# Performance work log

Measured on AMD Instinct MI355X. Metric: run time of the kernel, lower is better.

Reference implementation:

```python
import jax, jax.numpy as jnp
import numpy as np

D = 2048
H = 16
KV = 4
DH = D // H  # 128
REP = H // KV
ROPE_BASE = 10000.0


def _rope(x, pos):
    # x: (B, h, L, Dh), pos: (L,)
    half = x.shape[-1] // 2
    inv_freq = 1.0 / (ROPE_BASE ** (jnp.arange(0, half, dtype=jnp.float32) / half))
    ang = pos.astype(jnp.float32)[:, None] * inv_freq[None, :]          # (L, half)
    cos = jnp.concatenate([jnp.cos(ang), jnp.cos(ang)], axis=-1)        # (L, Dh)
    sin = jnp.concatenate([jnp.sin(ang), jnp.sin(ang)], axis=-1)
    x1, x2 = x[..., :half], x[..., half:]
    rot = jnp.concatenate([-x2, x1], axis=-1)
    return x * cos[None, None] + rot * sin[None, None]


def setup_inputs() -> dict:
    key = jax.random.key(0)
    ks = jax.random.split(key, 5)
    s = 1.0 / np.sqrt(D)
    return {
        "x": jax.random.normal(ks[0], (2, 2048, D), dtype=jnp.float32),
        "wq": jax.random.uniform(ks[1], (H * DH, D), jnp.float32, -s, s),
        "wk": jax.random.uniform(ks[2], (KV * DH, D), jnp.float32, -s, s),
        "wv": jax.random.uniform(ks[3], (KV * DH, D), jnp.float32, -s, s),
        "wo": jax.random.uniform(ks[4], (D, H * DH), jnp.float32, -s, s),
    }


def reference(x, wq, wk, wv, wo):
    B, T, _ = x.shape
    q = (x @ wq.T).reshape(B, T, H, DH).transpose(0, 2, 1, 3)    # (B,H,T,Dh)
    k = (x @ wk.T).reshape(B, T, KV, DH).transpose(0, 2, 1, 3)   # (B,KV,T,Dh)
    v = (x @ wv.T).reshape(B, T, KV, DH).transpose(0, 2, 1, 3)
    Tc = T  # no kv cache
    pos = jnp.arange(Tc)
    q = _rope(q, pos)
    k = _rope(k, pos)
    # GQA: repeat kv heads to match query heads
    k_full = jnp.repeat(k, REP, axis=1)                          # (B,H,Tc,Dh)
    v_full = jnp.repeat(v, REP, axis=1)
    scale = 1.0 / np.sqrt(DH)
    scores = jnp.einsum('bhtd,bhsd->bhts', q, k_full) * scale    # (B,H,T,Tc)
    row = jnp.arange(T)[:, None]
    col = jnp.arange(Tc)[None, :]
    causal = col <= row + (Tc - T)
    scores = jnp.where(causal[None, None], scores, -jnp.inf)
    attn = jax.nn.softmax(scores, axis=-1)
    out = jnp.einsum('bhts,bhsd->bhtd', attn, v_full)            # (B,H,T,Dh)
    out = out.transpose(0, 2, 1, 3).reshape(B, T, H * DH)
    return out @ wo.T
```

## Files before the change

kernel.cpp:

```cpp
#include <hip/hip_runtime.h>

typedef float f32x4 __attribute__((ext_vector_type(4)));
typedef short s16x8 __attribute__((ext_vector_type(8)));
typedef unsigned short u16;

__device__ __forceinline__ u16 f2bf(float f) {
    union { float f; unsigned u; } v; v.f = f;
    return (u16)((v.u + 0x7fffu + ((v.u >> 16) & 1u)) >> 16);
}
__device__ __forceinline__ float bf2f(u16 h) {
    union { unsigned u; float f; } v; v.u = ((unsigned)h) << 16;
    return v.f;
}
__device__ __forceinline__ float fast_exp2(float x) {
#if __has_builtin(__builtin_amdgcn_exp2f)
    return __builtin_amdgcn_exp2f(x);
#else
    return exp2f(x);
#endif
}

__device__ __forceinline__ void gload_lds16(const void* g, void* l) {
    __builtin_amdgcn_global_load_lds((__attribute__((address_space(1))) void*)g,
                                     (__attribute__((address_space(3))) void*)l, 16, 0, 0);
}

__global__ __launch_bounds__(256) void cvt_all(const float* __restrict__ x,  const float* __restrict__ wq,
                                               const float* __restrict__ wk, const float* __restrict__ wv,
                                               u16* __restrict__ xb, u16* __restrict__ wqkvb) {
    int u = blockIdx.x * 256 + threadIdx.x;
    const float* src;
    u16* dst;
    if (u < 1048576) { src = x + (size_t)u * 8; dst = xb + (size_t)u * 8; }
    else {
        int w = u - 1048576;
        dst = wqkvb + (size_t)w * 8;
        if (w < 524288)      src = wq + (size_t)w * 8;
        else if (w < 655360) src = wk + (size_t)(w - 524288) * 8;
        else                 src = wv + (size_t)(w - 655360) * 8;
    }
    const float4* p = (const float4*)src;
    float4 a = p[0], b = p[1];
    s16x8 o;
    o[0] = f2bf(a.x); o[1] = f2bf(a.y); o[2] = f2bf(a.z); o[3] = f2bf(a.w);
    o[4] = f2bf(b.x); o[5] = f2bf(b.y); o[6] = f2bf(b.z); o[7] = f2bf(b.w);
    *(s16x8*)dst = o;
}

__global__ __launch_bounds__(256) void cvt_kernel(const float* __restrict__ in,
                                                  u16* __restrict__ out, int n8) {
    int i = blockIdx.x * 256 + threadIdx.x;
    if (i >= n8) return;
    const float4* p = (const float4*)(in + (size_t)i * 8);
    float4 a = p[0], b = p[1];
    s16x8 o;
    o[0] = f2bf(a.x); o[1] = f2bf(a.y); o[2] = f2bf(a.z); o[3] = f2bf(a.w);
    o[4] = f2bf(b.x); o[5] = f2bf(b.y); o[6] = f2bf(b.z); o[7] = f2bf(b.w);
    *(s16x8*)(out + (size_t)i * 8) = o;
}

template<int OUT>
__global__ __launch_bounds__(256) void gemm128(const u16* __restrict__ A, const u16* __restrict__ B,
                                               void* __restrict__ C, void* __restrict__ Ck,
                                               void* __restrict__ Cv, int M, int N, int K) {
    __shared__ __align__(16) u16 Ald[128 * 64];
    __shared__ __align__(16) u16 Bld[128 * 64];
    const int t = threadIdx.x, wid = t >> 6, lane = t & 63;
    const int m0 = blockIdx.y * 128, n0 = blockIdx.x * 128;
    const int ml = lane & 15, quad = lane >> 4, m7 = ml & 7;
    const int wm = (wid & 1) * 64, wn = (wid >> 1) * 64;
    const int sr = lane >> 3, sc = lane & 7;

    f32x4 acc[4][4] = {};

    for (int k0 = 0; k0 < K; k0 += 64) {
        if (k0) __syncthreads();
        #pragma unroll
        for (int i = 0; i < 4; ++i) {
            int seg = wid * 4 + i;
            int r = seg * 8 + sr;
            int c = (sc ^ (r & 7)) * 8;
            gload_lds16(A + (size_t)(m0 + r) * K + k0 + c, &Ald[seg * 512]);
            gload_lds16(B + (size_t)(n0 + r) * K + k0 + c, &Bld[seg * 512]);
        }
        __syncthreads();
        #pragma unroll
        for (int kk = 0; kk < 64; kk += 32) {
            s16x8 af[4], bf[4];
            #pragma unroll
            for (int mi = 0; mi < 4; ++mi)
                af[mi] = *(const s16x8*)&Ald[(wm + mi * 16 + ml) * 64 + (((kk >> 3) + quad) ^ m7) * 8];
            #pragma unroll
            for (int ni = 0; ni < 4; ++ni)
                bf[ni] = *(const s16x8*)&Bld[(wn + ni * 16 + ml) * 64 + (((kk >> 3) + quad) ^ m7) * 8];
            #pragma unroll
            for (int mi = 0; mi < 4; ++mi)
                #pragma unroll
                for (int ni = 0; ni < 4; ++ni)
                    acc[mi][ni] = __builtin_amdgcn_mfma_f32_16x16x32_bf16(af[mi], bf[ni], acc[mi][ni], 0, 0, 0);
        }
    }
    #pragma unroll
    for (int mi = 0; mi < 4; ++mi)
        #pragma unroll
        for (int ni = 0; ni < 4; ++ni) {
            int gmb = m0 + wm + mi * 16 + quad * 4;
            int gn  = n0 + wn + ni * 16 + ml;
            if constexpr (OUT == 4) {
                if (n0 < 2048) {
                    #pragma unroll
                    for (int r = 0; r < 4; ++r)
                        ((u16*)C)[(size_t)(gmb + r) * 2048 + gn] = f2bf(acc[mi][ni][r]);
                } else if (n0 < 2560) {
                    #pragma unroll
                    for (int r = 0; r < 4; ++r)
                        ((u16*)Ck)[(size_t)(gmb + r) * 512 + (gn - 2048)] = f2bf(acc[mi][ni][r]);
                } else {
                    ushort4 v;
                    v.x = f2bf(acc[mi][ni][0]); v.y = f2bf(acc[mi][ni][1]);
                    v.z = f2bf(acc[mi][ni][2]); v.w = f2bf(acc[mi][ni][3]);
                    *(ushort4*)((u16*)Cv + (size_t)(gn - 2560) * M + gmb) = v;
                }
            } else {
                #pragma unroll
                for (int r = 0; r < 4; ++r)
                    ((float*)C)[(size_t)(gmb + r) * N + gn] = acc[mi][ni][r];
            }
        }
}

__global__ __launch_bounds__(256) void rope_kernel(u16* __restrict__ qb, u16* __restrict__ kb,
                                                   int nq, int ntot, float sq) {
    int idx = blockIdx.x * 256 + threadIdx.x;
    if (idx >= ntot) return;
    u16* base; int nheads; float scl; int id;
    if (idx < nq) { base = qb; nheads = 16; scl = sq;  id = idx; }
    else          { base = kb; nheads = 4;  scl = 1.f; id = idx - nq; }
    int i = id & 63;
    int rest = id >> 6;
    int hh = rest % nheads;
    int tok = rest / nheads;
    int tpos = tok & 2047;
    u16* row = base + (size_t)tok * nheads * 128 + hh * 128;
    float x1 = bf2f(row[i]);
    float x2 = bf2f(row[i + 64]);
    float inv = expf(-(float)i * 0.14391156731570787f);
    float ang = (float)tpos * inv;
    float s, c;
    sincosf(ang, &s, &c);
    row[i]      = f2bf((x1 * c - x2 * s) * scl);
    row[i + 64] = f2bf((x2 * c + x1 * s) * scl);
}

__global__ __launch_bounds__(256, 2) void attn_kernel(const u16* __restrict__ Q, const u16* __restrict__ Kb,
                                                      const u16* __restrict__ Vt, u16* __restrict__ O) {
    __shared__ __align__(16) u16 Klds[64 * 128];
    __shared__ __align__(16) u16 Vlds[128 * 64];
    __shared__ __align__(16) u16 Plds[4][2][16 * 64];
    const int t = threadIdx.x, wslot = t >> 6, lane = t & 63;
    const int qa = blockIdx.x, qb = 127 - (int)blockIdx.x;
    const int kv = blockIdx.y, b = blockIdx.z;
    const int h = kv * 4 + wslot;
    const int ml = lane & 15, quad = lane >> 4, m7 = ml & 7;
    const int t0a = qa * 16, t0b = qb * 16;

    s16x8 qfA[4], qfB[4];
    {
        const u16* qpA = Q + ((size_t)(b * 2048 + t0a + ml) * 2048 + h * 128);
        const u16* qpB = Q + ((size_t)(b * 2048 + t0b + ml) * 2048 + h * 128);
        #pragma unroll
        for (int kc = 0; kc < 4; ++kc) {
            qfA[kc] = *(const s16x8*)(qpA + kc * 32 + quad * 8);
            qfB[kc] = *(const s16x8*)(qpB + kc * 32 + quad * 8);
        }
    }

    s16x8 ones;
    #pragma unroll
    for (int j = 0; j < 8; ++j) ones[j] = (short)0x3F80;

    f32x4 OA[8] = {}, OB[8] = {};
    f32x4 LA = {}, LB = {};

    const int nsb = (qb >> 2) + 1;
    const int lastA = qa >> 2;

    for (int it = 0; it < nsb; ++it) {
        const int s0 = it * 64;
        if (it) __syncthreads();
        #pragma unroll
        for (int i = 0; i < 4; ++i) {
            int seg = wslot * 4 + i;
            int kr = seg * 4 + (lane >> 4);
            int kc = ((lane & 15) ^ (kr & 7)) * 8;
            gload_lds16(Kb + (size_t)(b * 2048 + s0 + kr) * 512 + kv * 128 + kc, &Klds[seg * 512]);
            int vr = seg * 8 + (lane >> 3);
            int vc = ((lane & 7) ^ (vr & 7)) * 8;
            gload_lds16(Vt + (size_t)(kv * 128 + vr) * 4096 + b * 2048 + s0 + vc, &Vlds[seg * 512]);
        }
        __syncthreads();

        const bool actA = (it <= lastA);

        f32x4 Sa[4] = {}, Sb[4] = {};
        if (actA) {
            #pragma unroll
            for (int kc = 0; kc < 4; ++kc)
                #pragma unroll
                for (int ti = 0; ti < 4; ++ti) {
                    s16x8 kf = *(const s16x8*)&Klds[(ti * 16 + ml) * 128 + ((kc * 4 + quad) ^ m7) * 8];
                    Sb[ti] = __builtin_amdgcn_mfma_f32_16x16x32_bf16(qfB[kc], kf, Sb[ti], 0, 0, 0);
                    Sa[ti] = __builtin_amdgcn_mfma_f32_16x16x32_bf16(qfA[kc], kf, Sa[ti], 0, 0, 0);
                }
        } else {
            #pragma unroll
            for (int kc = 0; kc < 4; ++kc)
                #pragma unroll
                for (int ti = 0; ti < 4; ++ti) {
                    s16x8 kf = *(const s16x8*)&Klds[(ti * 16 + ml) * 128 + ((kc * 4 + quad) ^ m7) * 8];
                    Sb[ti] = __builtin_amdgcn_mfma_f32_16x16x32_bf16(qfB[kc], kf, Sb[ti], 0, 0, 0);
                }
        }

        auto do_soft = [&](f32x4* S, int t0, int pslot) {
            u16* pl = &Plds[wslot][pslot][0];
            #pragma unroll
            for (int r = 0; r < 4; ++r) {
                int qr = t0 + quad * 4 + r;
                int row = quad * 4 + r;
                #pragma unroll
                for (int ti = 0; ti < 4; ++ti) {
                    float e = fast_exp2(S[ti][r]);
                    if (s0 + ti * 16 + ml > qr) e = 0.f;
                    union { float f; unsigned u; } cv; cv.f = e;
                    pl[row * 64 + (((ti * 2 + (ml >> 3)) ^ (row & 7)) * 8) + (ml & 7)] = (u16)(cv.u >> 16);
                }
            }
        };
        do_soft(Sb, t0b, 1);
        if (actA) do_soft(Sa, t0a, 0);
        asm volatile("s_waitcnt lgkmcnt(0)" ::: "memory");
        s16x8 pfA[2], pfB[2];
        pfB[0] = *(const s16x8*)&Plds[wslot][1][ml * 64 + ((quad)     ^ m7) * 8];
        pfB[1] = *(const s16x8*)&Plds[wslot][1][ml * 64 + ((4 + quad) ^ m7) * 8];
        if (actA) {
            pfA[0] = *(const s16x8*)&Plds[wslot][0][ml * 64 + ((quad)     ^ m7) * 8];
            pfA[1] = *(const s16x8*)&Plds[wslot][0][ml * 64 + ((4 + quad) ^ m7) * 8];
        }
        asm volatile("s_waitcnt lgkmcnt(0)" ::: "memory");

        if (actA) {
            #pragma unroll
            for (int c = 0; c < 2; ++c) {
                #pragma unroll
                for (int nt = 0; nt < 8; ++nt) {
                    s16x8 vf = *(const s16x8*)&Vlds[(nt * 16 + ml) * 64 + ((c * 4 + quad) ^ m7) * 8];
                    OB[nt] = __builtin_amdgcn_mfma_f32_16x16x32_bf16(pfB[c], vf, OB[nt], 0, 0, 0);
                    OA[nt] = __builtin_amdgcn_mfma_f32_16x16x32_bf16(pfA[c], vf, OA[nt], 0, 0, 0);
                }
                LB = __builtin_amdgcn_mfma_f32_16x16x32_bf16(pfB[c], ones, LB, 0, 0, 0);
                LA = __builtin_amdgcn_mfma_f32_16x16x32_bf16(pfA[c], ones, LA, 0, 0, 0);
            }
        } else {
            #pragma unroll
            for (int c = 0; c < 2; ++c) {
                #pragma unroll
                for (int nt = 0; nt < 8; ++nt) {
                    s16x8 vf = *(const s16x8*)&Vlds[(nt * 16 + ml) * 64 + ((c * 4 + quad) ^ m7) * 8];
                    OB[nt] = __builtin_amdgcn_mfma_f32_16x16x32_bf16(pfB[c], vf, OB[nt], 0, 0, 0);
                }
                LB = __builtin_amdgcn_mfma_f32_16x16x32_bf16(pfB[c], ones, LB, 0, 0, 0);
            }
        }
    }

    #pragma unroll
    for (int nt = 0; nt < 8; ++nt)
        #pragma unroll
        for (int r = 0; r < 4; ++r) {
            int col = h * 128 + nt * 16 + ml;
            O[(size_t)(b * 2048 + t0b + quad * 4 + r) * 2048 + col] = f2bf(OB[nt][r] / LB[r]);
            O[(size_t)(b * 2048 + t0a + quad * 4 + r) * 2048 + col] = f2bf(OA[nt][r] / LA[r]);
        }
}

extern "C" void kernel_launch(void* const* d_in, const int* in_sizes, int n_in,
                              void* d_out, int out_size, void* d_ws, size_t ws_size,
                              hipStream_t stream) {
    const float* x  = (const float*)d_in[0];
    const float* wq = (const float*)d_in[1];
    const float* wk = (const float*)d_in[2];
    const float* wv = (const float*)d_in[3];
    const float* wo = (const float*)d_in[4];
    float* out = (float*)d_out;
    char* ws = (char*)d_ws;

    const size_t MB = 1024 * 1024;
    u16* xb    = (u16*)(ws);
    u16* qb    = (u16*)(ws + 16 * MB);
    u16* kb    = (u16*)(ws + 32 * MB);
    u16* vtb   = (u16*)(ws + 36 * MB);
    u16* wqkvb = (u16*)(ws + 40 * MB);
    u16* ab    = xb;
    u16* wob   = wqkvb;

    cvt_all<<<7168, 256, 0, stream>>>(x, wq, wk, wv, xb, wqkvb);

    gemm128<4><<<dim3(24, 32), 256, 0, stream>>>(xb, wqkvb, qb, kb, vtb, 4096, 3072, 2048);

    cvt_kernel<<<2048, 256, 0, stream>>>(wo, wob, 524288);

    rope_kernel<<<20480, 256, 0, stream>>>(qb, kb, 4194304, 5242880, 0.12751743f);

    attn_kernel<<<dim3(64, 4, 2), 256, 0, stream>>>(qb, kb, vtb, ab);

    gemm128<1><<<dim3(16, 32), 256, 0, stream>>>(ab, wob, out, nullptr, nullptr, 4096, 2048, 2048);
}
```

Before: 336.0 us.

## Split paired query tiles into one tile per block with staggered ordering

The attention kernel no longer gives each block a pair of complementary query tiles (qa, 127-qa) for load balance. Each block now handles a single 16-row query tile, the grid doubles to 128 blocks in x, and the tile order is permuted per (kv,batch) group to spread long and short tiles across the machine. Launch bounds go from 2 to 4 blocks per SIMD-group target, and the causal mask is applied only on the diagonal iteration. This raises block count and occupancy and cuts register pressure. In exchange, K/V tiles loaded into LDS are reused by one query tile instead of two, so shared-memory load traffic per MFMA roughly doubles.

```diff
diff --git a/kernel.cpp b/kernel.cpp
--- a/kernel.cpp
+++ b/kernel.cpp
@@ -152,40 +152,43 @@
     row[i + 64] = f2bf((x2 * c + x1 * s) * scl);
 }
 
-__global__ __launch_bounds__(256, 2) void attn_kernel(const u16* __restrict__ Q, const u16* __restrict__ Kb,
+__global__ __launch_bounds__(256, 4) void attn_kernel(const u16* __restrict__ Q, const u16* __restrict__ Kb,
                                                       const u16* __restrict__ Vt, u16* __restrict__ O) {
     __shared__ __align__(16) u16 Klds[64 * 128];
     __shared__ __align__(16) u16 Vlds[128 * 64];
-    __shared__ __align__(16) u16 Plds[4][2][16 * 64];
+    __shared__ __align__(16) u16 Plds[4][16 * 64];
     const int t = threadIdx.x, wslot = t >> 6, lane = t & 63;
-    const int qa = blockIdx.x, qb = 127 - (int)blockIdx.x;
     const int kv = blockIdx.y, b = blockIdx.z;
+    const int g = kv + 4 * b;
+    const int bx = blockIdx.x;
+    int qt;
+    switch ((g >> 1) & 3) {
+        case 0:  qt = bx; break;
+        case 1:  qt = 127 - bx; break;
+        case 2:  qt = (bx + 64) & 127; break;
+        default: qt = (63 - bx) & 127; break;
+    }
     const int h = kv * 4 + wslot;
     const int ml = lane & 15, quad = lane >> 4, m7 = ml & 7;
-    const int t0a = qa * 16, t0b = qb * 16;
-
-    s16x8 qfA[4], qfB[4];
+    const int t0 = qt * 16;
+    const int n = (qt >> 2) + 1;
+
+    s16x8 qf[4];
     {
-        const u16* qpA = Q + ((size_t)(b * 2048 + t0a + ml) * 2048 + h * 128);
-        const u16* qpB = Q + ((size_t)(b * 2048 + t0b + ml) * 2048 + h * 128);
-        #pragma unroll
-        for (int kc = 0; kc < 4; ++kc) {
-            qfA[kc] = *(const s16x8*)(qpA + kc * 32 + quad * 8);
-            qfB[kc] = *(const s16x8*)(qpB + kc * 32 + quad * 8);
-        }
+        const u16* qp = Q + ((size_t)(b * 2048 + t0 + ml) * 2048 + h * 128);
+        #pragma unroll
+        for (int kc = 0; kc < 4; ++kc)
+            qf[kc] = *(const s16x8*)(qp + kc * 32 + quad * 8);
     }
 
     s16x8 ones;
     #pragma unroll
     for (int j = 0; j < 8; ++j) ones[j] = (short)0x3F80;
 
-    f32x4 OA[8] = {}, OB[8] = {};
-    f32x4 LA = {}, LB = {};
-
-    const int nsb = (qb >> 2) + 1;
-    const int lastA = qa >> 2;
-
-    for (int it = 0; it < nsb; ++it) {
+    f32x4 Oa[8] = {};
+    f32x4 L = {};
+
+    for (int it = 0; it < n; ++it) {
         const int s0 = it * 64;
         if (it) __syncthreads();
         #pragma unroll
@@ -200,30 +203,18 @@
         }
         __syncthreads();
 
-        const bool actA = (it <= lastA);
-
-        f32x4 Sa[4] = {}, Sb[4] = {};
-        if (actA) {
-            #pragma unroll
-            for (int kc = 0; kc < 4; ++kc)
-                #pragma unroll
-                for (int ti = 0; ti < 4; ++ti) {
-                    s16x8 kf = *(const s16x8*)&Klds[(ti * 16 + ml) * 128 + ((kc * 4 + quad) ^ m7) * 8];
-                    Sb[ti] = __builtin_amdgcn_mfma_f32_16x16x32_bf16(qfB[kc], kf, Sb[ti], 0, 0, 0);
-                    Sa[ti] = __builtin_amdgcn_mfma_f32_16x16x32_bf16(qfA[kc], kf, Sa[ti], 0, 0, 0);
-                }
-        } else {
-            #pragma unroll
-            for (int kc = 0; kc < 4; ++kc)
-                #pragma unroll
-                for (int ti = 0; ti < 4; ++ti) {
-                    s16x8 kf = *(const s16x8*)&Klds[(ti * 16 + ml) * 128 + ((kc * 4 + quad) ^ m7) * 8];
-                    Sb[ti] = __builtin_amdgcn_mfma_f32_16x16x32_bf16(qfB[kc], kf, Sb[ti], 0, 0, 0);
-                }
-        }
-
-        auto do_soft = [&](f32x4* S, int t0, int pslot) {
-            u16* pl = &Plds[wslot][pslot][0];
+        f32x4 S[4] = {};
+        #pragma unroll
+        for (int kc = 0; kc < 4; ++kc)
+            #pragma unroll
+            for (int ti = 0; ti < 4; ++ti) {
+                s16x8 kf = *(const s16x8*)&Klds[(ti * 16 + ml) * 128 + ((kc * 4 + quad) ^ m7) * 8];
+                S[ti] = __builtin_amdgcn_mfma_f32_16x16x32_bf16(qf[kc], kf, S[ti], 0, 0, 0);
+            }
+
+        {
+            u16* pl = &Plds[wslot][0];
+            const bool diag = (it == n - 1);
             #pragma unroll
             for (int r = 0; r < 4; ++r) {
                 int qr = t0 + quad * 4 + r;
@@ -231,46 +222,26 @@
                 #pragma unroll
                 for (int ti = 0; ti < 4; ++ti) {
                     float e = fast_exp2(S[ti][r]);
-                    if (s0 + ti * 16 + ml > qr) e = 0.f;
+                    if (diag && (s0 + ti * 16 + ml > qr)) e = 0.f;
                     union { float f; unsigned u; } cv; cv.f = e;
                     pl[row * 64 + (((ti * 2 + (ml >> 3)) ^ (row & 7)) * 8) + (ml & 7)] = (u16)(cv.u >> 16);
                 }
             }
-        };
-        do_soft(Sb, t0b, 1);
-        if (actA) do_soft(Sa, t0a, 0);
+        }
         asm volatile("s_waitcnt lgkmcnt(0)" ::: "memory");
-        s16x8 pfA[2], pfB[2];
-        pfB[0] = *(const s16x8*)&Plds[wslot][1][ml * 64 + ((quad)     ^ m7) * 8];
-        pfB[1] = *(const s16x8*)&Plds[wslot][1][ml * 64 + ((4 + quad) ^ m7) * 8];
-        if (actA) {
-            pfA[0] = *(const s16x8*)&Plds[wslot][0][ml * 64 + ((quad)     ^ m7) * 8];
-            pfA[1] = *(const s16x8*)&Plds[wslot][0][ml * 64 + ((4 + quad) ^ m7) * 8];
-        }
+        s16x8 pf[2];
+        pf[0] = *(const s16x8*)&Plds[wslot][ml * 64 + ((quad)     ^ m7) * 8];
+        pf[1] = *(const s16x8*)&Plds[wslot][ml * 64 + ((4 + quad) ^ m7) * 8];
         asm volatile("s_waitcnt lgkmcnt(0)" ::: "memory");
 
-        if (actA) {
-            #pragma unroll
-            for (int c = 0; c < 2; ++c) {
-                #pragma unroll
-                for (int nt = 0; nt < 8; ++nt) {
-                    s16x8 vf = *(const s16x8*)&Vlds[(nt * 16 + ml) * 64 + ((c * 4 + quad) ^ m7) * 8];
-                    OB[nt] = __builtin_amdgcn_mfma_f32_16x16x32_bf16(pfB[c], vf, OB[nt], 0, 0, 0);
-                    OA[nt] = __builtin_amdgcn_mfma_f32_16x16x32_bf16(pfA[c], vf, OA[nt], 0, 0, 0);
-                }
-                LB = __builtin_amdgcn_mfma_f32_16x16x32_bf16(pfB[c], ones, LB, 0, 0, 0);
-                LA = __builtin_amdgcn_mfma_f32_16x16x32_bf16(pfA[c], ones, LA, 0, 0, 0);
-            }
-        } else {
-            #pragma unroll
-            for (int c = 0; c < 2; ++c) {
-                #pragma unroll
-                for (int nt = 0; nt < 8; ++nt) {
-                    s16x8 vf = *(const s16x8*)&Vlds[(nt * 16 + ml) * 64 + ((c * 4 + quad) ^ m7) * 8];
-                    OB[nt] = __builtin_amdgcn_mfma_f32_16x16x32_bf16(pfB[c], vf, OB[nt], 0, 0, 0);
-                }
-                LB = __builtin_amdgcn_mfma_f32_16x16x32_bf16(pfB[c], ones, LB, 0, 0, 0);
-            }
+        #pragma unroll
+        for (int c = 0; c < 2; ++c) {
+            #pragma unroll
+            for (int nt = 0; nt < 8; ++nt) {
+                s16x8 vf = *(const s16x8*)&Vlds[(nt * 16 + ml) * 64 + ((c * 4 + quad) ^ m7) * 8];
+                Oa[nt] = __builtin_amdgcn_mfma_f32_16x16x32_bf16(pf[c], vf, Oa[nt], 0, 0, 0);
+            }
+            L = __builtin_amdgcn_mfma_f32_16x16x32_bf16(pf[c], ones, L, 0, 0, 0);
         }
     }
 
@@ -279,8 +250,7 @@
         #pragma unroll
         for (int r = 0; r < 4; ++r) {
             int col = h * 128 + nt * 16 + ml;
-            O[(size_t)(b * 2048 + t0b + quad * 4 + r) * 2048 + col] = f2bf(OB[nt][r] / LB[r]);
-            O[(size_t)(b * 2048 + t0a + quad * 4 + r) * 2048 + col] = f2bf(OA[nt][r] / LA[r]);
+            O[(size_t)(b * 2048 + t0 + quad * 4 + r) * 2048 + col] = f2bf(Oa[nt][r] / L[r]);
         }
 }
 
@@ -312,7 +282,7 @@
 
     rope_kernel<<<20480, 256, 0, stream>>>(qb, kb, 4194304, 5242880, 0.12751743f);
 
-    attn_kernel<<<dim3(64, 4, 2), 256, 0, stream>>>(qb, kb, vtb, ab);
+    attn_kernel<<<dim3(128, 4, 2), 256, 0, stream>>>(qb, kb, vtb, ab);
 
     gemm128<1><<<dim3(16, 32), 256, 0, stream>>>(ab, wob, out, nullptr, nullptr, 4096, 2048, 2048);
 }
```

Measured after the change: 334.6 us. No clear change (-0.4%).

## Load K/V fragments directly from global memory instead of staging through LDS

Applied to the files above, without the earlier changes.

The attention kernel stops cooperatively staging K and V tiles into shared memory and drops the per-iteration block barriers. Each wave now reads its K and V MFMA fragments straight from global memory, relying on L1/L2 for reuse across the four waves of a block. The grid is flattened so the 8 (kv, batch) groups sharing a query-tile index are interleaved, which should improve cache locality, and the causal mask is applied only on the diagonal tile. The trade is more global load instructions and redundant per-wave traffic in exchange for removing LDS round trips and synchronisation.

```diff
diff --git a/kernel.cpp b/kernel.cpp
--- a/kernel.cpp
+++ b/kernel.cpp
@@ -154,15 +154,18 @@
 
 __global__ __launch_bounds__(256, 2) void attn_kernel(const u16* __restrict__ Q, const u16* __restrict__ Kb,
                                                       const u16* __restrict__ Vt, u16* __restrict__ O) {
-    __shared__ __align__(16) u16 Klds[64 * 128];
-    __shared__ __align__(16) u16 Vlds[128 * 64];
     __shared__ __align__(16) u16 Plds[4][2][16 * 64];
     const int t = threadIdx.x, wslot = t >> 6, lane = t & 63;
-    const int qa = blockIdx.x, qb = 127 - (int)blockIdx.x;
-    const int kv = blockIdx.y, b = blockIdx.z;
+    const int bid = blockIdx.x;
+    const int g = bid & 7;
+    const int u = bid >> 3;
+    const int kv = g & 3, b = g >> 2;
+    const int qa = u, qb = 127 - u;
     const int h = kv * 4 + wslot;
     const int ml = lane & 15, quad = lane >> 4, m7 = ml & 7;
     const int t0a = qa * 16, t0b = qb * 16;
+    const int na = (qa >> 2) + 1;
+    const int nb = (qb >> 2) + 1;
 
     s16x8 qfA[4], qfB[4];
     {
@@ -182,25 +185,12 @@
     f32x4 OA[8] = {}, OB[8] = {};
     f32x4 LA = {}, LB = {};
 
-    const int nsb = (qb >> 2) + 1;
-    const int lastA = qa >> 2;
-
-    for (int it = 0; it < nsb; ++it) {
+    const u16* kfb = Kb + (size_t)(b * 2048 + ml) * 512 + kv * 128 + quad * 8;
+    const u16* vfb = Vt + (size_t)(kv * 128 + ml) * 4096 + b * 2048 + quad * 8;
+
+    for (int it = 0; it < nb; ++it) {
         const int s0 = it * 64;
-        if (it) __syncthreads();
-        #pragma unroll
-        for (int i = 0; i < 4; ++i) {
-            int seg = wslot * 4 + i;
-            int kr = seg * 4 + (lane >> 4);
-            int kc = ((lane & 15) ^ (kr & 7)) * 8;
-            gload_lds16(Kb + (size_t)(b * 2048 + s0 + kr) * 512 + kv * 128 + kc, &Klds[seg * 512]);
-            int vr = seg * 8 + (lane >> 3);
-            int vc = ((lane & 7) ^ (vr & 7)) * 8;
-            gload_lds16(Vt + (size_t)(kv * 128 + vr) * 4096 + b * 2048 + s0 + vc, &Vlds[seg * 512]);
-        }
-        __syncthreads();
-
-        const bool actA = (it <= lastA);
+        const bool actA = (it < na);
 
         f32x4 Sa[4] = {}, Sb[4] = {};
         if (actA) {
@@ -208,7 +198,7 @@
             for (int kc = 0; kc < 4; ++kc)
                 #pragma unroll
                 for (int ti = 0; ti < 4; ++ti) {
-                    s16x8 kf = *(const s16x8*)&Klds[(ti * 16 + ml) * 128 + ((kc * 4 + quad) ^ m7) * 8];
+                    s16x8 kf = *(const s16x8*)(kfb + (size_t)(s0 + ti * 16) * 512 + kc * 32);
                     Sb[ti] = __builtin_amdgcn_mfma_f32_16x16x32_bf16(qfB[kc], kf, Sb[ti], 0, 0, 0);
                     Sa[ti] = __builtin_amdgcn_mfma_f32_16x16x32_bf16(qfA[kc], kf, Sa[ti], 0, 0, 0);
                 }
@@ -217,12 +207,12 @@
             for (int kc = 0; kc < 4; ++kc)
                 #pragma unroll
                 for (int ti = 0; ti < 4; ++ti) {
-                    s16x8 kf = *(const s16x8*)&Klds[(ti * 16 + ml) * 128 + ((kc * 4 + quad) ^ m7) * 8];
+                    s16x8 kf = *(const s16x8*)(kfb + (size_t)(s0 + ti * 16) * 512 + kc * 32);
                     Sb[ti] = __builtin_amdgcn_mfma_f32_16x16x32_bf16(qfB[kc], kf, Sb[ti], 0, 0, 0);
                 }
         }
 
-        auto do_soft = [&](f32x4* S, int t0, int pslot) {
+        auto do_soft = [&](f32x4* S, int t0, int pslot, bool diag) {
             u16* pl = &Plds[wslot][pslot][0];
             #pragma unroll
             for (int r = 0; r < 4; ++r) {
@@ -231,14 +221,14 @@
                 #pragma unroll
                 for (int ti = 0; ti < 4; ++ti) {
                     float e = fast_exp2(S[ti][r]);
-                    if (s0 + ti * 16 + ml > qr) e = 0.f;
+                    if (diag && (s0 + ti * 16 + ml > qr)) e = 0.f;
                     union { float f; unsigned u; } cv; cv.f = e;
                     pl[row * 64 + (((ti * 2 + (ml >> 3)) ^ (row & 7)) * 8) + (ml & 7)] = (u16)(cv.u >> 16);
                 }
             }
         };
-        do_soft(Sb, t0b, 1);
-        if (actA) do_soft(Sa, t0a, 0);
+        do_soft(Sb, t0b, 1, it == nb - 1);
+        if (actA) do_soft(Sa, t0a, 0, it == na - 1);
         asm volatile("s_waitcnt lgkmcnt(0)" ::: "memory");
         s16x8 pfA[2], pfB[2];
         pfB[0] = *(const s16x8*)&Plds[wslot][1][ml * 64 + ((quad)     ^ m7) * 8];
@@ -254,7 +244,7 @@
             for (int c = 0; c < 2; ++c) {
                 #pragma unroll
                 for (int nt = 0; nt < 8; ++nt) {
-                    s16x8 vf = *(const s16x8*)&Vlds[(nt * 16 + ml) * 64 + ((c * 4 + quad) ^ m7) * 8];
+                    s16x8 vf = *(const s16x8*)(vfb + (size_t)(nt * 16) * 4096 + s0 + c * 32);
                     OB[nt] = __builtin_amdgcn_mfma_f32_16x16x32_bf16(pfB[c], vf, OB[nt], 0, 0, 0);
                     OA[nt] = __builtin_amdgcn_mfma_f32_16x16x32_bf16(pfA[c], vf, OA[nt], 0, 0, 0);
                 }
@@ -266,7 +256,7 @@
             for (int c = 0; c < 2; ++c) {
                 #pragma unroll
                 for (int nt = 0; nt < 8; ++nt) {
-                    s16x8 vf = *(const s16x8*)&Vlds[(nt * 16 + ml) * 64 + ((c * 4 + quad) ^ m7) * 8];
+                    s16x8 vf = *(const s16x8*)(vfb + (size_t)(nt * 16) * 4096 + s0 + c * 32);
                     OB[nt] = __builtin_amdgcn_mfma_f32_16x16x32_bf16(pfB[c], vf, OB[nt], 0, 0, 0);
                 }
                 LB = __builtin_amdgcn_mfma_f32_16x16x32_bf16(pfB[c], ones, LB, 0, 0, 0);
@@ -312,7 +302,7 @@
 
     rope_kernel<<<20480, 256, 0, stream>>>(qb, kb, 4194304, 5242880, 0.12751743f);
 
-    attn_kernel<<<dim3(64, 4, 2), 256, 0, stream>>>(qb, kb, vtb, ab);
+    attn_kernel<<<512, 256, 0, stream>>>(qb, kb, vtb, ab);
 
     gemm128<1><<<dim3(16, 32), 256, 0, stream>>>(ab, wob, out, nullptr, nullptr, 4096, 2048, 2048);
 }
```

New measurement: 425.2 us. +26.5%, slower.
